# Performance work log

Hardware: AMD Instinct MI355X
Metric: run time of the kernel (lower is better)

The kernel has to match this reference:

```python
import jax, jax.numpy as jnp
import numpy as np

N_NODES = 50000
N_EDGES = 200000
D_FEAT = 364
D_OUT = 150
N_PAIRS = 8192
NEG_SLOPE = 0.01
EPS = 1e-12


def setup_inputs() -> dict:
    key = jax.random.key(0)
    ks = jax.random.split(key, 12)
    features = jax.random.normal(ks[0], (N_NODES, D_FEAT), dtype=jnp.float32)
    src = jax.random.randint(ks[1], (N_EDGES,), 0, N_NODES)
    dst = jax.random.randint(ks[2], (N_EDGES,), 0, N_NODES)
    v1 = jax.random.randint(ks[3], (N_PAIRS,), 0, N_NODES)
    v2 = jax.random.randint(ks[4], (N_PAIRS,), 0, N_NODES)
    s = 1.0 / np.sqrt(D_FEAT)
    W1 = jax.random.normal(ks[5], (D_FEAT, D_FEAT), dtype=jnp.float32) * s
    b1 = jax.random.normal(ks[6], (D_FEAT,), dtype=jnp.float32) * s
    W2 = jax.random.normal(ks[7], (D_FEAT, D_FEAT), dtype=jnp.float32) * s
    b2 = jax.random.normal(ks[8], (D_FEAT,), dtype=jnp.float32) * s
    W3 = jax.random.normal(ks[9], (D_FEAT, D_OUT), dtype=jnp.float32) * s
    b3 = jax.random.normal(ks[10], (D_OUT,), dtype=jnp.float32) * s
    return {"features": features, "src": src, "dst": dst, "v1": v1, "v2": v2,
            "W1": W1, "b1": b1, "W2": W2, "b2": b2, "W3": W3, "b3": b3}


def _gcn_sum_layer(x, src, dst, W, b):
    # DGL copy_u/sum: each dst node sums src features over incoming edges.
    agg = jax.ops.segment_sum(x[src], dst, num_segments=N_NODES)  # [N, D]
    h = agg + x  # residual
    return h @ W + b


def _l2_normalize(x):
    norm = jnp.sqrt(jnp.sum(x * x, axis=1, keepdims=True))
    return x / jnp.maximum(norm, EPS)


def reference(features, src, dst, v1, v2, W1, b1, W2, b2, W3, b3):
    lrelu = lambda x: jax.nn.leaky_relu(x, negative_slope=NEG_SLOPE)
    gcn = lrelu(_gcn_sum_layer(features, src, dst, W1, b1))
    gcn = lrelu(_gcn_sum_layer(gcn, src, dst, W2, b2))
    z1 = _l2_normalize(lrelu(gcn[v1] @ W3 + b3))
    z2 = _l2_normalize(lrelu(gcn[v2] @ W3 + b3))
    return (z1, z2)
```

## Files before the change

### kernel.cpp

```cpp
#include <hip/hip_runtime.h>

#define NN 50000
#define NE 200000
#define DF 364
#define KP 384
#define DOUT 150
#define NP 8192
#define NEG_SLOPE 0.01f

typedef float f32x4 __attribute__((ext_vector_type(4)));
typedef short bf16x8 __attribute__((ext_vector_type(8)));
typedef unsigned short u16x8 __attribute__((ext_vector_type(8)));

__device__ __forceinline__ unsigned short f2bf(float x) {
    unsigned u = __float_as_uint(x);
    u += 0x7FFF + ((u >> 16) & 1);
    return (unsigned short)(u >> 16);
}
__device__ __forceinline__ float bf2f(unsigned short h) {
    return __uint_as_float(((unsigned)h) << 16);
}

__device__ __forceinline__ void mfma16(f32x4& d, bf16x8 a, bf16x8 b) {
    d = __builtin_amdgcn_mfma_f32_16x16x32_bf16(a, b, d, 0, 0, 0);
}



__global__ void hist_kernel(const int* __restrict__ dst, int* __restrict__ deg, int n) {
    int t = blockIdx.x * blockDim.x + threadIdx.x;
    if (t < n) atomicAdd(&deg[dst[t]], 1);
}

__global__ __launch_bounds__(1024) void scan_block(const int* __restrict__ deg,
                                                   int* __restrict__ rowptr,
                                                   int* __restrict__ bsum, int n) {
    __shared__ int lds[1024];
    int b = blockIdx.x, t = threadIdx.x;
    int i = b * 1024 + t;
    int v = (i < n) ? deg[i] : 0;
    lds[t] = v;
    __syncthreads();
    for (int off = 1; off < 1024; off <<= 1) {
        int x = (t >= off) ? lds[t - off] : 0;
        __syncthreads();
        lds[t] += x;
        __syncthreads();
    }
    if (i < n) rowptr[i] = lds[t] - v;
    if (t == 1023) bsum[b] = lds[1023];
}

__global__ void scan_small(int* __restrict__ bsum, int nb) {
    int t = threadIdx.x;
    int orig = (t < nb) ? bsum[t] : 0;
    int v = orig;
#pragma unroll
    for (int off = 1; off < 64; off <<= 1) {
        int u = __shfl_up(v, off, 64);
        if (t >= off) v += u;
    }
    if (t < nb) bsum[t] = v - orig;
}

__global__ __launch_bounds__(1024) void add_off(int* __restrict__ rowptr,
                                                const int* __restrict__ bsum,
                                                int* __restrict__ pos, int n) {
    int i = blockIdx.x * 1024 + threadIdx.x;
    if (i < n) {
        int v = rowptr[i] + bsum[blockIdx.x];
        rowptr[i] = v;
        pos[i] = v;
    }
}

__global__ void fill_kernel(const int* __restrict__ src, const int* __restrict__ dst,
                            int* __restrict__ pos, int* __restrict__ esrc, int n) {
    int t = blockIdx.x * blockDim.x + threadIdx.x;
    if (t < n) {
        int j = atomicAdd(&pos[dst[t]], 1);
        esrc[j] = src[t];
    }
}


__device__ __forceinline__ void f4add(float4& a, const float4 b) {
    a.x += b.x; a.y += b.y; a.z += b.z; a.w += b.w;
}

__device__ __forceinline__ ushort4 round4(float4 v) {
    ushort4 h;
    h.x = f2bf(v.x); h.y = f2bf(v.y); h.z = f2bf(v.z); h.w = f2bf(v.w);
    return h;
}

__device__ __forceinline__ size_t frag_off_lo(int g, int rr, int i) {
    return (size_t)(g * 12 + (i >> 3)) * 512 + ((i >> 1) & 3) * 128 + rr * 8 + (i & 1) * 4;
}
__device__ __forceinline__ size_t frag_off_hi(int g, int rr, int i) {
    return (size_t)(g * 12 + 8 + (i >> 3)) * 512 + ((i >> 1) & 3) * 128 + rr * 8 + (i & 1) * 4;
}


__global__ __launch_bounds__(256) void agg1_kernel(
    const float* __restrict__ x, const int* __restrict__ rowptr,
    const int* __restrict__ deg, const int* __restrict__ esrc,
    ushort* __restrict__ of, int nrows) {
    int wid = (blockIdx.x * 256 + threadIdx.x) >> 6;
    if (wid >= nrows) return;
    int lane = threadIdx.x & 63;
    int start = rowptr[wid];
    int d = deg[wid];
    bool hi2 = lane < 27;

    const float4* xr = reinterpret_cast<const float4*>(x + (size_t)wid * DF);
    float4 a0 = xr[lane];
    float4 a1 = hi2 ? xr[64 + lane] : make_float4(0.f, 0.f, 0.f, 0.f);

    int j = 0;
    for (; j + 1 < d; j += 2) {
        int s0 = esrc[start + j], s1 = esrc[start + j + 1];
        const float4* r0 = reinterpret_cast<const float4*>(x + (size_t)s0 * DF);
        const float4* r1 = reinterpret_cast<const float4*>(x + (size_t)s1 * DF);
        float4 b0 = r0[lane], b1 = r1[lane];
        f4add(a0, b0);
        f4add(a0, b1);
        if (hi2) {
            float4 c0 = r0[64 + lane], c1 = r1[64 + lane];
            f4add(a1, c0);
            f4add(a1, c1);
        }
    }
    if (j < d) {
        int s0 = esrc[start + j];
        const float4* r0 = reinterpret_cast<const float4*>(x + (size_t)s0 * DF);
        f4add(a0, r0[lane]);
        if (hi2) f4add(a1, r0[64 + lane]);
    }

    int g = wid >> 4, rr = wid & 15;
    *(ushort4*)&of[frag_off_lo(g, rr, lane)] = round4(a0);
    if (lane < 32) {
        float4 v = hi2 ? a1 : make_float4(0.f, 0.f, 0.f, 0.f);
        *(ushort4*)&of[frag_off_hi(g, rr, lane)] = round4(v);
    }
}


__global__ __launch_bounds__(256) void agg2_kernel(
    const ushort* __restrict__ h1, const int* __restrict__ rowptr,
    const int* __restrict__ deg, const int* __restrict__ esrc,
    const int* __restrict__ v1, const int* __restrict__ v2,
    ushort* __restrict__ of, int nrows) {
    int wid = (blockIdx.x * 256 + threadIdx.x) >> 6;
    if (wid >= nrows) return;
    int lane = threadIdx.x & 63;
    int node = (wid < NP) ? v1[wid] : v2[wid - NP];
    int start = rowptr[node];
    int d = deg[node];
    bool act = lane < 48;

    float f[8] = {};
    if (act) {
        u16x8 v = *(const u16x8*)&h1[(size_t)node * KP + lane * 8];
#pragma unroll
        for (int i = 0; i < 8; ++i) f[i] = bf2f(v[i]);
    }
    for (int j = 0; j < d; ++j) {
        int s = esrc[start + j];
        if (act) {
            u16x8 v = *(const u16x8*)&h1[(size_t)s * KP + lane * 8];
#pragma unroll
            for (int i = 0; i < 8; ++i) f[i] += bf2f(v[i]);
        }
    }
    if (act) {
        u16x8 o;
#pragma unroll
        for (int i = 0; i < 8; ++i) o[i] = f2bf(f[i]);
        int g = wid >> 4, rr = wid & 15;
        size_t off = (size_t)(g * 12 + (lane >> 2)) * 512 + (lane & 3) * 128 + rr * 8;
        *(u16x8*)&of[off] = o;
    }
}


__global__ void prep_w(const float* __restrict__ W, int K, int Nn,
                       ushort* __restrict__ th, ushort* __restrict__ tl) {
    int idx = blockIdx.x * 256 + threadIdx.x;
    if (idx >= KP * KP) return;
    int e = idx & 7;
    int rr = (idx >> 3) & 15;
    int sub = (idx >> 7) & 3;
    int gc = idx >> 9;
    int g = gc / 12, c = gc - g * 12;
    int k = c * 32 + sub * 8 + e;
    int n = g * 16 + rr;
    float v = (k < K && n < Nn) ? W[(size_t)k * Nn + n] : 0.f;
    unsigned short h = f2bf(v);
    th[idx] = h;
    tl[idx] = f2bf(v - bf2f(h));
}


__global__ __launch_bounds__(256, 3) void gemm_lds(
    const ushort* __restrict__ Af, const ushort* __restrict__ Bhf,
    const ushort* __restrict__ Blf, const float* __restrict__ bias,
    ushort* __restrict__ Cbf, float* __restrict__ Cf32,
    int M, int Nn, int mode) {
    __shared__ __align__(16) ushort lds[2][3][4096];

    int tid = threadIdx.x;
    int lane = tid & 63;
    int wv = tid >> 6;
    int wr = wv >> 1, wc = wv & 1;
    int brow = blockIdx.x * 128, bcol = blockIdx.y * 128;
    int rg = brow >> 4, cg = bcol >> 4;

#define STAGE(buf, tt)                                                                  \
    do {                                                                                \
        _Pragma("unroll") for (int j_ = 0; j_ < 6; ++j_) {                              \
            int g24_ = wv * 6 + j_;                                                     \
            int p_ = g24_ >> 3, gg_ = g24_ & 7;                                         \
            const ushort* base_ = (p_ == 0) ? Af : ((p_ == 1) ? Bhf : Blf);             \
            int grp_ = ((p_ == 0) ? rg : cg) + gg_;                                     \
            const ushort* s_ = base_ + ((size_t)grp_ * 12 + (tt)) * 512 + lane * 8;     \
            __builtin_amdgcn_global_load_lds(                                           \
                (const __attribute__((address_space(1))) unsigned int*)s_,              \
                (__attribute__((address_space(3))) unsigned int*)(&lds[buf][p_][gg_ * 512]), \
                16, 0, 0);                                                              \
        }                                                                               \
    } while (0)

    int flo = (lane >> 4) * 128 + (lane & 15) * 8;

    f32x4 acc[4][4];
#pragma unroll
    for (int m = 0; m < 4; ++m)
#pragma unroll
        for (int n = 0; n < 4; ++n) acc[m][n] = (f32x4){0.f, 0.f, 0.f, 0.f};

    STAGE(0, 0);
    __syncthreads();

    for (int t = 0; t < KP / 32; ++t) {
        int cur = t & 1;
        if (t + 1 < KP / 32) STAGE(1 - cur, t + 1);
        bf16x8 a[4], bh[4], bl[4];
#pragma unroll
        for (int m = 0; m < 4; ++m)
            a[m] = *(const bf16x8*)&lds[cur][0][(wr * 4 + m) * 512 + flo];
#pragma unroll
        for (int n = 0; n < 4; ++n) {
            bh[n] = *(const bf16x8*)&lds[cur][1][(wc * 4 + n) * 512 + flo];
            bl[n] = *(const bf16x8*)&lds[cur][2][(wc * 4 + n) * 512 + flo];
        }
#pragma unroll
        for (int m = 0; m < 4; ++m)
#pragma unroll
            for (int n = 0; n < 4; ++n) {
                mfma16(acc[m][n], a[m], bh[n]);
                mfma16(acc[m][n], a[m], bl[n]);
            }
        __syncthreads();
    }
#undef STAGE

    int crow_l = (lane >> 4) * 4;
    int ccol_l = lane & 15;
#pragma unroll
    for (int n = 0; n < 4; ++n) {
        int col = bcol + wc * 64 + n * 16 + ccol_l;
        bool cok = (col < Nn);
        float bn = cok ? bias[col] : 0.f;
#pragma unroll
        for (int m = 0; m < 4; ++m) {
#pragma unroll
            for (int r = 0; r < 4; ++r) {
                int row = brow + wr * 64 + m * 16 + crow_l + r;
                if (row >= M) continue;
                float v = acc[m][n][r] + bn;
                v = (v >= 0.f) ? v : NEG_SLOPE * v;
                if (mode == 2) {
                    if (cok) Cf32[(size_t)row * Nn + col] = v;
                } else {
                    unsigned short h = cok ? f2bf(v) : (unsigned short)0;
                    size_t off;
                    if (mode == 0) {
                        off = (size_t)row * KP + col;
                    } else {
                        off = (size_t)((row >> 4) * 12 + (col >> 5)) * 512 +
                              ((col >> 3) & 3) * 128 + (row & 15) * 8 + (col & 7);
                    }
                    Cbf[off] = h;
                }
            }
        }
    }
}


__global__ __launch_bounds__(256) void norm_kernel(float* __restrict__ out, int nrows) {
    int wid = (blockIdx.x * 256 + threadIdx.x) >> 6;
    if (wid >= nrows) return;
    int lane = threadIdx.x & 63;
    float* row = out + (size_t)wid * DOUT;
    float a = row[lane];
    float b = row[lane + 64];
    float cc = (lane + 128 < DOUT) ? row[lane + 128] : 0.f;
    float s = a * a + b * b + cc * cc;
#pragma unroll
    for (int off = 32; off; off >>= 1) s += __shfl_xor(s, off, 64);
    float scale = 1.0f / fmaxf(sqrtf(s), 1e-12f);
    row[lane] = a * scale;
    row[lane + 64] = b * scale;
    if (lane + 128 < DOUT) row[lane + 128] = cc * scale;
}


extern "C" void kernel_launch(void* const* d_in, const int* in_sizes, int n_in,
                              void* d_out, int out_size, void* d_ws, size_t ws_size,
                              hipStream_t stream) {
    const float* features = (const float*)d_in[0];
    const int* src = (const int*)d_in[1];
    const int* dst = (const int*)d_in[2];
    const int* v1 = (const int*)d_in[3];
    const int* v2 = (const int*)d_in[4];
    const float* W1 = (const float*)d_in[5];
    const float* b1 = (const float*)d_in[6];
    const float* W2 = (const float*)d_in[7];
    const float* b2 = (const float*)d_in[8];
    const float* W3 = (const float*)d_in[9];
    const float* b3 = (const float*)d_in[10];
    float* out = (float*)d_out;

    const int MPAD = 50048;
    const size_t PLANE = (size_t)MPAD * KP;
    const size_t WSZ = (size_t)KP * KP;

    char* p = (char*)d_ws;
    ushort* a1f = (ushort*)p; p += PLANE * 2;
    ushort* h1 = (ushort*)p; p += PLANE * 2;
    ushort* wt1h = (ushort*)p; p += WSZ * 2;
    ushort* wt1l = (ushort*)p; p += WSZ * 2;
    ushort* wt2h = (ushort*)p; p += WSZ * 2;
    ushort* wt2l = (ushort*)p; p += WSZ * 2;
    ushort* wt3h = (ushort*)p; p += WSZ * 2;
    ushort* wt3l = (ushort*)p; p += WSZ * 2;
    int* deg = (int*)p; p += NN * 4;
    int* rowptr = (int*)p; p += NN * 4;
    int* pos = (int*)p; p += NN * 4;
    int* esrc = (int*)p; p += NE * 4;
    int* bsum = (int*)p; p += 256;
    ushort* a2f = a1f;
    ushort* h2f = h1;

    const int NSB = (NN + 1023) / 1024;

    hipMemsetAsync(deg, 0, NN * sizeof(int), stream);
    hist_kernel<<<(NE + 255) / 256, 256, 0, stream>>>(dst, deg, NE);
    scan_block<<<NSB, 1024, 0, stream>>>(deg, rowptr, bsum, NN);
    scan_small<<<1, 64, 0, stream>>>(bsum, NSB);
    add_off<<<NSB, 1024, 0, stream>>>(rowptr, bsum, pos, NN);
    fill_kernel<<<(NE + 255) / 256, 256, 0, stream>>>(src, dst, pos, esrc, NE);

    prep_w<<<(KP * KP + 255) / 256, 256, 0, stream>>>(W1, DF, DF, wt1h, wt1l);
    prep_w<<<(KP * KP + 255) / 256, 256, 0, stream>>>(W2, DF, DF, wt2h, wt2l);
    prep_w<<<(KP * KP + 255) / 256, 256, 0, stream>>>(W3, DF, DOUT, wt3h, wt3l);

    agg1_kernel<<<(NN * 64 + 255) / 256, 256, 0, stream>>>(features, rowptr, deg, esrc,
                                                           a1f, NN);
    gemm_lds<<<dim3(391, 3), 256, 0, stream>>>(a1f, wt1h, wt1l, b1,
                                               h1, nullptr, NN, DF, 0);

    const int NR = 2 * NP;
    agg2_kernel<<<(NR * 64 + 255) / 256, 256, 0, stream>>>(h1, rowptr, deg, esrc,
                                                           v1, v2, a2f, NR);
    gemm_lds<<<dim3(128, 3), 256, 0, stream>>>(a2f, wt2h, wt2l, b2,
                                               h2f, nullptr, NR, DF, 1);

    gemm_lds<<<dim3(128, 2), 256, 0, stream>>>(h2f, wt3h, wt3l, b3,
                                               nullptr, out, NR, DOUT, 2);
    norm_kernel<<<(NR * 64 + 255) / 256, 256, 0, stream>>>(out, NR);
}
```

Measured before the change: 349.5 us.

## Pre-convert features to bf16 and transpose GEMM roles for vectorized epilogue stores

```diff
diff --git a/kernel.cpp b/kernel.cpp
--- a/kernel.cpp
+++ b/kernel.cpp
@@ -84,16 +84,20 @@
 }
 
 
-__device__ __forceinline__ void f4add(float4& a, const float4 b) {
-    a.x += b.x; a.y += b.y; a.z += b.z; a.w += b.w;
-}
-
 __device__ __forceinline__ ushort4 round4(float4 v) {
     ushort4 h;
     h.x = f2bf(v.x); h.y = f2bf(v.y); h.z = f2bf(v.z); h.w = f2bf(v.w);
     return h;
 }
 
+__device__ __forceinline__ float4 bf4tof4(ushort4 u) {
+    return make_float4(bf2f(u.x), bf2f(u.y), bf2f(u.z), bf2f(u.w));
+}
+
+__device__ __forceinline__ void f4add(float4& a, const float4 b) {
+    a.x += b.x; a.y += b.y; a.z += b.z; a.w += b.w;
+}
+
 __device__ __forceinline__ size_t frag_off_lo(int g, int rr, int i) {
     return (size_t)(g * 12 + (i >> 3)) * 512 + ((i >> 1) & 3) * 128 + rr * 8 + (i & 1) * 4;
 }
@@ -102,8 +106,18 @@
 }
 
 
+__global__ __launch_bounds__(256) void feat2bf(const float* __restrict__ x,
+                                               ushort* __restrict__ o, int n4) {
+    int i = blockIdx.x * 256 + threadIdx.x;
+    if (i < n4) {
+        float4 v = *(const float4*)&x[(size_t)i * 4];
+        *(ushort4*)&o[(size_t)i * 4] = round4(v);
+    }
+}
+
+
 __global__ __launch_bounds__(256) void agg1_kernel(
-    const float* __restrict__ x, const int* __restrict__ rowptr,
+    const ushort* __restrict__ xb, const int* __restrict__ rowptr,
     const int* __restrict__ deg, const int* __restrict__ esrc,
     ushort* __restrict__ of, int nrows) {
     int wid = (blockIdx.x * 256 + threadIdx.x) >> 6;
@@ -113,29 +127,32 @@
     int d = deg[wid];
     bool hi2 = lane < 27;
 
-    const float4* xr = reinterpret_cast<const float4*>(x + (size_t)wid * DF);
-    float4 a0 = xr[lane];
-    float4 a1 = hi2 ? xr[64 + lane] : make_float4(0.f, 0.f, 0.f, 0.f);
+    const ushort* xr = xb + (size_t)wid * DF;
+    float4 a0 = bf4tof4(*(const ushort4*)&xr[4 * lane]);
+    float4 a1 = hi2 ? bf4tof4(*(const ushort4*)&xr[256 + 4 * lane])
+                    : make_float4(0.f, 0.f, 0.f, 0.f);
 
     int j = 0;
     for (; j + 1 < d; j += 2) {
         int s0 = esrc[start + j], s1 = esrc[start + j + 1];
-        const float4* r0 = reinterpret_cast<const float4*>(x + (size_t)s0 * DF);
-        const float4* r1 = reinterpret_cast<const float4*>(x + (size_t)s1 * DF);
-        float4 b0 = r0[lane], b1 = r1[lane];
-        f4add(a0, b0);
-        f4add(a0, b1);
+        const ushort* r0 = xb + (size_t)s0 * DF;
+        const ushort* r1 = xb + (size_t)s1 * DF;
+        ushort4 b0 = *(const ushort4*)&r0[4 * lane];
+        ushort4 b1 = *(const ushort4*)&r1[4 * lane];
+        f4add(a0, bf4tof4(b0));
+        f4add(a0, bf4tof4(b1));
         if (hi2) {
-            float4 c0 = r0[64 + lane], c1 = r1[64 + lane];
-            f4add(a1, c0);
-            f4add(a1, c1);
+            ushort4 c0 = *(const ushort4*)&r0[256 + 4 * lane];
+            ushort4 c1 = *(const ushort4*)&r1[256 + 4 * lane];
+            f4add(a1, bf4tof4(c0));
+            f4add(a1, bf4tof4(c1));
         }
     }
     if (j < d) {
         int s0 = esrc[start + j];
-        const float4* r0 = reinterpret_cast<const float4*>(x + (size_t)s0 * DF);
-        f4add(a0, r0[lane]);
-        if (hi2) f4add(a1, r0[64 + lane]);
+        const ushort* r0 = xb + (size_t)s0 * DF;
+        f4add(a0, bf4tof4(*(const ushort4*)&r0[4 * lane]));
+        if (hi2) f4add(a1, bf4tof4(*(const ushort4*)&r0[256 + 4 * lane]));
     }
 
     int g = wid >> 4, rr = wid & 15;
@@ -204,10 +221,10 @@
 
 
 __global__ __launch_bounds__(256, 3) void gemm_lds(
-    const ushort* __restrict__ Af, const ushort* __restrict__ Bhf,
-    const ushort* __restrict__ Blf, const float* __restrict__ bias,
+    const ushort* __restrict__ Awh, const ushort* __restrict__ Awl,
+    const ushort* __restrict__ Bact, const float* __restrict__ bias,
     ushort* __restrict__ Cbf, float* __restrict__ Cf32,
-    int M, int Nn, int mode) {
+    int Nrow, int mode) {
     __shared__ __align__(16) ushort lds[2][3][4096];
 
     int tid = threadIdx.x;
@@ -222,8 +239,8 @@
         _Pragma("unroll") for (int j_ = 0; j_ < 6; ++j_) {                              \
             int g24_ = wv * 6 + j_;                                                     \
             int p_ = g24_ >> 3, gg_ = g24_ & 7;                                         \
-            const ushort* base_ = (p_ == 0) ? Af : ((p_ == 1) ? Bhf : Blf);             \
-            int grp_ = ((p_ == 0) ? rg : cg) + gg_;                                     \
+            const ushort* base_ = (p_ == 0) ? Awh : ((p_ == 1) ? Awl : Bact);           \
+            int grp_ = ((p_ == 2) ? cg : rg) + gg_;                                     \
             const ushort* s_ = base_ + ((size_t)grp_ * 12 + (tt)) * 512 + lane * 8;     \
             __builtin_amdgcn_global_load_lds(                                           \
                 (const __attribute__((address_space(1))) unsigned int*)s_,              \
@@ -246,21 +263,21 @@
     for (int t = 0; t < KP / 32; ++t) {
         int cur = t & 1;
         if (t + 1 < KP / 32) STAGE(1 - cur, t + 1);
-        bf16x8 a[4], bh[4], bl[4];
+        bf16x8 ah[4], al[4], b[4];
+#pragma unroll
+        for (int m = 0; m < 4; ++m) {
+            ah[m] = *(const bf16x8*)&lds[cur][0][(wr * 4 + m) * 512 + flo];
+            al[m] = *(const bf16x8*)&lds[cur][1][(wr * 4 + m) * 512 + flo];
+        }
+#pragma unroll
+        for (int n = 0; n < 4; ++n)
+            b[n] = *(const bf16x8*)&lds[cur][2][(wc * 4 + n) * 512 + flo];
 #pragma unroll
         for (int m = 0; m < 4; ++m)
-            a[m] = *(const bf16x8*)&lds[cur][0][(wr * 4 + m) * 512 + flo];
-#pragma unroll
-        for (int n = 0; n < 4; ++n) {
-            bh[n] = *(const bf16x8*)&lds[cur][1][(wc * 4 + n) * 512 + flo];
-            bl[n] = *(const bf16x8*)&lds[cur][2][(wc * 4 + n) * 512 + flo];
-        }
-#pragma unroll
-        for (int m = 0; m < 4; ++m)
 #pragma unroll
             for (int n = 0; n < 4; ++n) {
-                mfma16(acc[m][n], a[m], bh[n]);
-                mfma16(acc[m][n], a[m], bl[n]);
+                mfma16(acc[m][n], ah[m], b[n]);
+                mfma16(acc[m][n], al[m], b[n]);
             }
         __syncthreads();
     }
@@ -269,30 +286,44 @@
     int crow_l = (lane >> 4) * 4;
     int ccol_l = lane & 15;
 #pragma unroll
-    for (int n = 0; n < 4; ++n) {
-        int col = bcol + wc * 64 + n * 16 + ccol_l;
-        bool cok = (col < Nn);
-        float bn = cok ? bias[col] : 0.f;
-#pragma unroll
-        for (int m = 0; m < 4; ++m) {
+    for (int m = 0; m < 4; ++m) {
+        int rb = brow + wr * 64 + m * 16 + crow_l;
+        float bq[4];
+        if (rb + 3 < Nrow) {
+            float4 t = *(const float4*)&bias[rb];
+            bq[0] = t.x; bq[1] = t.y; bq[2] = t.z; bq[3] = t.w;
+        } else {
+#pragma unroll
+            for (int r = 0; r < 4; ++r) bq[r] = (rb + r < Nrow) ? bias[rb + r] : 0.f;
+        }
+#pragma unroll
+        for (int n = 0; n < 4; ++n) {
+            int col = bcol + wc * 64 + n * 16 + ccol_l;
+            float v[4];
 #pragma unroll
             for (int r = 0; r < 4; ++r) {
-                int row = brow + wr * 64 + m * 16 + crow_l + r;
-                if (row >= M) continue;
-                float v = acc[m][n][r] + bn;
-                v = (v >= 0.f) ? v : NEG_SLOPE * v;
-                if (mode == 2) {
-                    if (cok) Cf32[(size_t)row * Nn + col] = v;
+                float x = acc[m][n][r] + bq[r];
+                v[r] = (x >= 0.f) ? x : NEG_SLOPE * x;
+            }
+            if (mode == 0) {
+                ushort4 h;
+                h.x = f2bf(v[0]); h.y = f2bf(v[1]); h.z = f2bf(v[2]); h.w = f2bf(v[3]);
+                *(ushort4*)&Cbf[(size_t)col * KP + rb] = h;
+            } else if (mode == 1) {
+                ushort4 h;
+                h.x = f2bf(v[0]); h.y = f2bf(v[1]); h.z = f2bf(v[2]); h.w = f2bf(v[3]);
+                size_t off = ((size_t)(col >> 4) * 12 + (rb >> 5)) * 512 +
+                             ((rb >> 3) & 3) * 128 + (col & 15) * 8 + (rb & 7);
+                *(ushort4*)&Cbf[off] = h;
+            } else {
+                float* op = Cf32 + (size_t)col * DOUT + rb;
+                if (rb + 3 < Nrow) {
+                    *(float2*)op = make_float2(v[0], v[1]);
+                    *(float2*)(op + 2) = make_float2(v[2], v[3]);
                 } else {
-                    unsigned short h = cok ? f2bf(v) : (unsigned short)0;
-                    size_t off;
-                    if (mode == 0) {
-                        off = (size_t)row * KP + col;
-                    } else {
-                        off = (size_t)((row >> 4) * 12 + (col >> 5)) * 512 +
-                              ((col >> 3) & 3) * 128 + (row & 15) * 8 + (col & 7);
-                    }
-                    Cbf[off] = h;
+#pragma unroll
+                    for (int r = 0; r < 4; ++r)
+                        if (rb + r < Nrow) op[r] = v[r];
                 }
             }
         }
@@ -341,6 +372,7 @@
     char* p = (char*)d_ws;
     ushort* a1f = (ushort*)p; p += PLANE * 2;
     ushort* h1 = (ushort*)p; p += PLANE * 2;
+    ushort* fbf = (ushort*)p; p += (size_t)NN * DF * 2;
     ushort* wt1h = (ushort*)p; p += WSZ * 2;
     ushort* wt1l = (ushort*)p; p += WSZ * 2;
     ushort* wt2h = (ushort*)p; p += WSZ * 2;
@@ -353,7 +385,7 @@
     int* esrc = (int*)p; p += NE * 4;
     int* bsum = (int*)p; p += 256;
     ushort* a2f = a1f;
-    ushort* h2f = h1;
+    ushort* h2t = h1;
 
     const int NSB = (NN + 1023) / 1024;
 
@@ -364,22 +396,23 @@
     add_off<<<NSB, 1024, 0, stream>>>(rowptr, bsum, pos, NN);
     fill_kernel<<<(NE + 255) / 256, 256, 0, stream>>>(src, dst, pos, esrc, NE);
 
+    feat2bf<<<(NN * DF / 4 + 255) / 256, 256, 0, stream>>>(features, fbf, NN * DF / 4);
     prep_w<<<(KP * KP + 255) / 256, 256, 0, stream>>>(W1, DF, DF, wt1h, wt1l);
     prep_w<<<(KP * KP + 255) / 256, 256, 0, stream>>>(W2, DF, DF, wt2h, wt2l);
     prep_w<<<(KP * KP + 255) / 256, 256, 0, stream>>>(W3, DF, DOUT, wt3h, wt3l);
 
-    agg1_kernel<<<(NN * 64 + 255) / 256, 256, 0, stream>>>(features, rowptr, deg, esrc,
+    agg1_kernel<<<(NN * 64 + 255) / 256, 256, 0, stream>>>(fbf, rowptr, deg, esrc,
                                                            a1f, NN);
-    gemm_lds<<<dim3(391, 3), 256, 0, stream>>>(a1f, wt1h, wt1l, b1,
-                                               h1, nullptr, NN, DF, 0);
+    gemm_lds<<<dim3(3, 391), 256, 0, stream>>>(wt1h, wt1l, a1f, b1,
+                                               h1, nullptr, DF, 0);
 
     const int NR = 2 * NP;
     agg2_kernel<<<(NR * 64 + 255) / 256, 256, 0, stream>>>(h1, rowptr, deg, esrc,
                                                            v1, v2, a2f, NR);
-    gemm_lds<<<dim3(128, 3), 256, 0, stream>>>(a2f, wt2h, wt2l, b2,
-                                               h2f, nullptr, NR, DF, 1);
-
-    gemm_lds<<<dim3(128, 2), 256, 0, stream>>>(h2f, wt3h, wt3l, b3,
-                                               nullptr, out, NR, DOUT, 2);
+    gemm_lds<<<dim3(3, 128), 256, 0, stream>>>(wt2h, wt2l, a2f, b2,
+                                               h2t, nullptr, DF, 1);
+
+    gemm_lds<<<dim3(2, 128), 256, 0, stream>>>(wt3h, wt3l, h2t, b3,
+                                               nullptr, out, DOUT, 2);
     norm_kernel<<<(NR * 64 + 255) / 256, 256, 0, stream>>>(out, NR);
 }
```

After: 302.7 us. -13.4%, faster.
